# Optimization experiments

Measured on AMD Instinct MI355X. Metric: run time of the kernel, lower is better.

The kernel has to match this reference:

```python
import jax, jax.numpy as jnp
import numpy as np
from jax import lax


def setup_inputs() -> dict:
    key = jax.random.key(0)
    k1, k2, k3, k4 = jax.random.split(key, 4)
    B, C_in, H, W = 16, 64, 256, 256
    E, C_out, KH, KW = 4, 64, 3, 3
    inputs = jax.random.normal(k1, (B, C_in, H, W), dtype=jnp.float32)
    weight = jax.random.normal(k2, (E, C_out, C_in, KH, KW), dtype=jnp.float32) * 0.05
    fc_w = jax.random.normal(k3, (E, C_in), dtype=jnp.float32) * 0.1
    fc_b = jax.random.normal(k4, (E,), dtype=jnp.float32) * 0.1
    return {
        "inputs": inputs,
        "weight": weight,
        "fc_w": fc_w,
        "fc_b": fc_b,
        "stride": 1,
        "dilation": 1,
        "padding": 1,
    }


def reference(inputs, weight, fc_w, fc_b, stride, dilation, padding):
    # inputs: [B, C_in, H, W]; weight: [E, C_out, C_in, KH, KW]
    # Routing: adaptive avg pool to 1x1 == spatial mean, then Linear -> sigmoid.
    # (Dropout is identity in eval mode.)
    pooled = jnp.mean(inputs, axis=(2, 3))                      # [B, C_in]
    routing = jax.nn.sigmoid(pooled @ fc_w.T + fc_b)            # [B, E]
    # Per-sample mixed kernels.
    kernels = jnp.einsum("be,eoikl->boikl", routing, weight)    # [B, C_out, C_in, KH, KW]

    def conv_one(x, k):
        # x: [C_in, H, W], k: [C_out, C_in, KH, KW]
        y = lax.conv_general_dilated(
            x[None],
            k,
            window_strides=(stride, stride),
            padding=[(padding, padding), (padding, padding)],
            rhs_dilation=(dilation, dilation),
            dimension_numbers=("NCHW", "OIHW", "NCHW"),
        )
        return y[0]

    return jax.vmap(conv_one)(inputs, kernels)                  # [B, C_out, H', W']
```

## Files before the change

kernel.cpp:

```cpp
#include <hip/hip_runtime.h>
#include <math.h>

#define B_   16
#define CIN  64
#define COUT 64
#define H_   256
#define W_   256

typedef short s16x8  __attribute__((ext_vector_type(8)));
typedef float f32x16 __attribute__((ext_vector_type(16)));

__device__ __forceinline__ void split_bf16(float v, unsigned short& hi, unsigned short& lo) {
    unsigned u = __float_as_uint(v);
    hi = (unsigned short)(u >> 16);
    float hif = __uint_as_float(u & 0xffff0000u);
    lo = (unsigned short)(__float_as_uint(v - hif) >> 16);
}

__global__ __launch_bounds__(256) void pool_kernel(const float* __restrict__ x,
                                                   float* __restrict__ pooled) {
    const int plane = blockIdx.x;
    const float4* p = (const float4*)(x + (size_t)plane * (H_ * W_));
    float s = 0.f;
    for (int i = threadIdx.x; i < (H_ * W_) / 4; i += 256) {
        float4 v = p[i];
        s += (v.x + v.y) + (v.z + v.w);
    }
    #pragma unroll
    for (int off = 32; off > 0; off >>= 1) s += __shfl_down(s, off);
    __shared__ float red[4];
    if ((threadIdx.x & 63) == 0) red[threadIdx.x >> 6] = s;
    __syncthreads();
    if (threadIdx.x == 0)
        pooled[plane] = (red[0] + red[1] + red[2] + red[3]) * (1.f / (H_ * W_));
}

__global__ void routing_kernel(const float* __restrict__ pooled,
                               const float* __restrict__ fc_w,
                               const float* __restrict__ fc_b,
                               float* __restrict__ routing) {
    const int tid = threadIdx.x;
    const int b = tid >> 2, e = tid & 3;
    float s = fc_b[e];
    for (int c = 0; c < CIN; ++c) s += pooled[b * CIN + c] * fc_w[e * CIN + c];
    routing[b * 4 + e] = 1.f / (1.f + expf(-s));
}

__global__ __launch_bounds__(256) void mix_kernel(const float* __restrict__ routing,
                                                  const float* __restrict__ weight,
                                                  unsigned short* __restrict__ mixed) {
    const int gid = blockIdx.x * 256 + threadIdx.x;
    const int icL = gid & 15;
    const int oc  = (gid >> 4) & 63;
    const int q   = (gid >> 10) & 3;
    const int b   = gid >> 12;
    const int ic  = q * 16 + icL;

    float r[4];
    #pragma unroll
    for (int e = 0; e < 4; ++e) r[e] = routing[b * 4 + e];

    float s[9];
    #pragma unroll
    for (int t = 0; t < 9; ++t) s[t] = 0.f;
    #pragma unroll
    for (int e = 0; e < 4; ++e) {
        const float* wp = weight + (((size_t)e * COUT + oc) * CIN + ic) * 9;
        #pragma unroll
        for (int t = 0; t < 9; ++t) s[t] = fmaf(r[e], wp[t], s[t]);
    }
    unsigned short* base = mixed + (size_t)(b * 4 + q) * 18432;
    const int mb = oc >> 5;
    const int l  = (oc & 31) + ((icL >> 3) << 5);
    const int j  = icL & 7;
    #pragma unroll
    for (int t = 0; t < 9; ++t) {
        unsigned short hi, lo;
        split_bf16(s[t], hi, lo);
        base[(t * 4 + 0 + mb) * 512 + l * 8 + j] = hi;
        base[(t * 4 + 2 + mb) * 512 + l * 8 + j] = lo;
    }
}

__global__ __launch_bounds__(256, 3) void conv_kernel(const float* __restrict__ x,
                                                      const unsigned short* __restrict__ wmix,
                                                      float* __restrict__ y) {
    __shared__ __align__(16) unsigned short in_hi[10 * 34 * 16];
    __shared__ __align__(16) unsigned short in_lo[10 * 34 * 16];

    const int tid  = threadIdx.x;
    const int lane = tid & 63;
    const int wv   = tid >> 6;
    const int n    = lane & 31;
    const int kseg = lane >> 5;

    const int w0 = blockIdx.x * 32;
    const int h0 = blockIdx.y * 8;
    const int b  = blockIdx.z;

    const int p0 = tid;
    const int r0 = p0 / 34, c0 = p0 - r0 * 34;
    const int p1 = tid + 256;
    const int r1 = p1 / 34, c1 = p1 - r1 * 34;
    const bool has1 = (p1 < 340);

    const int gh0 = h0 - 1 + r0, gw0 = w0 - 1 + c0;
    const int gh1 = h0 - 1 + r1, gw1 = w0 - 1 + c1;
    const bool ok0 = ((unsigned)gh0 < H_) && ((unsigned)gw0 < W_);
    const bool ok1 = has1 && ((unsigned)gh1 < H_) && ((unsigned)gw1 < W_);

    const float* xb = x + (size_t)b * CIN * H_ * W_;
    const float* g0 = xb + (ok0 ? (gh0 * W_ + gw0) : 0);
    const float* g1 = xb + (ok1 ? (gh1 * W_ + gw1) : 0);

    float xr0[16], xr1[16];

    #define LOAD16(dst, gp, okf, qq) do {                                   \
        const float* _p = (gp) + (size_t)(qq) * 16 * (H_ * W_);             \
        _Pragma("unroll")                                                   \
        for (int _i = 0; _i < 16; ++_i)                                     \
            dst[_i] = (okf) ? _p[(size_t)_i * (H_ * W_)] : 0.f;             \
    } while (0)

    #define STAGE(pp, regs) do {                                            \
        s16x8 _vh0, _vh1, _vl0, _vl1;                                       \
        _Pragma("unroll")                                                   \
        for (int _i = 0; _i < 8; ++_i) {                                    \
            unsigned short _h, _l;                                          \
            split_bf16(regs[_i], _h, _l);                                   \
            _vh0[_i] = (short)_h; _vl0[_i] = (short)_l;                     \
            split_bf16(regs[8 + _i], _h, _l);                               \
            _vh1[_i] = (short)_h; _vl1[_i] = (short)_l;                     \
        }                                                                   \
        const int _c0 = (pp) * 2, _c1 = (pp) * 2 + 1;                       \
        const int _s0 = _c0 ^ ((_c0 >> 3) & 7);                             \
        const int _s1 = _c1 ^ ((_c1 >> 3) & 7);                             \
        ((s16x8*)in_hi)[_s0] = _vh0; ((s16x8*)in_hi)[_s1] = _vh1;           \
        ((s16x8*)in_lo)[_s0] = _vl0; ((s16x8*)in_lo)[_s1] = _vl1;           \
    } while (0)

    f32x16 acc[2][2];
    #pragma unroll
    for (int mb = 0; mb < 2; ++mb)
        #pragma unroll
        for (int nb = 0; nb < 2; ++nb)
            #pragma unroll
            for (int j = 0; j < 16; ++j) acc[mb][nb][j] = 0.f;

    const unsigned short* wb = wmix + (size_t)b * 4 * 18432 + lane * 8;

    LOAD16(xr0, g0, ok0, 0);
    if (has1) LOAD16(xr1, g1, ok1, 0);

    #pragma unroll 1
    for (int q = 0; q < 4; ++q) {
        __syncthreads();
        STAGE(p0, xr0);
        if (has1) STAGE(p1, xr1);
        __syncthreads();
        if (q < 3) {
            LOAD16(xr0, g0, ok0, q + 1);
            if (has1) LOAD16(xr1, g1, ok1, q + 1);
        }
        const unsigned short* wq = wb + q * 18432;

        s16x8 aH[2][2], aL[2][2];
        #pragma unroll
        for (int mb = 0; mb < 2; ++mb) {
            aH[0][mb] = *(const s16x8*)(wq + (0 + mb) * 512);
            aL[0][mb] = *(const s16x8*)(wq + (2 + mb) * 512);
        }
        #pragma unroll
        for (int tap = 0; tap < 9; ++tap) {
            const int cur = tap & 1, nxt = cur ^ 1;
            if (tap < 8) {
                #pragma unroll
                for (int mb = 0; mb < 2; ++mb) {
                    aH[nxt][mb] = *(const s16x8*)(wq + ((tap + 1) * 4 + 0 + mb) * 512);
                    aL[nxt][mb] = *(const s16x8*)(wq + ((tap + 1) * 4 + 2 + mb) * 512);
                }
            }
            const int kh = tap / 3, kw = tap - kh * 3;
            #pragma unroll
            for (int nb = 0; nb < 2; ++nb) {
                const int rin = wv * 2 + nb + kh;
                const int c   = (rin * 34 + n + kw) * 2 + kseg;
                const int cs  = c ^ ((c >> 3) & 7);
                const s16x8 bhi = ((const s16x8*)in_hi)[cs];
                const s16x8 blo = ((const s16x8*)in_lo)[cs];
                #pragma unroll
                for (int mb = 0; mb < 2; ++mb) {
                    acc[mb][nb] = __builtin_amdgcn_mfma_f32_32x32x16_bf16(aH[cur][mb], bhi, acc[mb][nb], 0, 0, 0);
                    acc[mb][nb] = __builtin_amdgcn_mfma_f32_32x32x16_bf16(aL[cur][mb], bhi, acc[mb][nb], 0, 0, 0);
                    acc[mb][nb] = __builtin_amdgcn_mfma_f32_32x32x16_bf16(aH[cur][mb], blo, acc[mb][nb], 0, 0, 0);
                }
            }
        }
    }

    #pragma unroll
    for (int mb = 0; mb < 2; ++mb) {
        #pragma unroll
        for (int nb = 0; nb < 2; ++nb) {
            const int hrow = h0 + wv * 2 + nb;
            #pragma unroll
            for (int r = 0; r < 16; ++r) {
                const int oc = mb * 32 + (r & 3) + 8 * (r >> 2) + 4 * kseg;
                y[(((size_t)b * COUT + oc) * H_ + hrow) * W_ + w0 + n] = acc[mb][nb][r];
            }
        }
    }
}

extern "C" void kernel_launch(void* const* d_in, const int* in_sizes, int n_in,
                              void* d_out, int out_size, void* d_ws, size_t ws_size,
                              hipStream_t stream) {
    const float* x      = (const float*)d_in[0];
    const float* weight = (const float*)d_in[1];
    const float* fc_w   = (const float*)d_in[2];
    const float* fc_b   = (const float*)d_in[3];
    float* out = (float*)d_out;

    float* ws      = (float*)d_ws;
    float* pooled  = ws;
    float* routing = ws + 1024;
    unsigned short* mixed = (unsigned short*)(ws + 1088);

    pool_kernel<<<B_ * CIN, 256, 0, stream>>>(x, pooled);
    routing_kernel<<<1, 64, 0, stream>>>(pooled, fc_w, fc_b, routing);
    mix_kernel<<<(B_ * 4 * COUT * 16) / 256, 256, 0, stream>>>(routing, weight, mixed);

    dim3 grid(W_ / 32, H_ / 8, B_);
    conv_kernel<<<grid, 256, 0, stream>>>(x, mixed, out);
}
```

Measured before the change: 644.9 us.

## Reuse LDS rows across kh taps, remap grid for XCD locality, drop prefetch

Restructures the conv inner loop by kw so the four input rows read from LDS are reused across all three kh taps, cutting LDS reads. The LDS layout becomes planar (hi/lo by k-segment) without the XOR swizzle. A 1D grid is remapped so consecutive blocks on each XCD cover adjacent tiles of the same batch. The register prefetch of the next channel group is removed and occupancy bounds drop from 3 to 2 waves per EU, which frees registers but exposes global load latency and may add LDS bank conflicts.

After: 640.2 us. No clear change (-0.7%).

```diff
diff --git a/kernel.cpp b/kernel.cpp
--- a/kernel.cpp
+++ b/kernel.cpp
@@ -82,11 +82,10 @@
     }
 }
 
-__global__ __launch_bounds__(256, 3) void conv_kernel(const float* __restrict__ x,
+__global__ __launch_bounds__(256, 2) void conv_kernel(const float* __restrict__ x,
                                                       const unsigned short* __restrict__ wmix,
                                                       float* __restrict__ y) {
-    __shared__ __align__(16) unsigned short in_hi[10 * 34 * 16];
-    __shared__ __align__(16) unsigned short in_lo[10 * 34 * 16];
+    __shared__ __align__(16) unsigned short in_s[4 * 340 * 8];
 
     const int tid  = threadIdx.x;
     const int lane = tid & 63;
@@ -94,9 +93,11 @@
     const int n    = lane & 31;
     const int kseg = lane >> 5;
 
-    const int w0 = blockIdx.x * 32;
-    const int h0 = blockIdx.y * 8;
-    const int b  = blockIdx.z;
+    const int bid = blockIdx.x;
+    const int wg  = (bid & 7) * 512 + (bid >> 3);
+    const int w0 = (wg & 7) * 32;
+    const int h0 = ((wg >> 3) & 31) * 8;
+    const int b  = wg >> 8;
 
     const int p0 = tid;
     const int r0 = p0 / 34, c0 = p0 - r0 * 34;
@@ -112,8 +113,6 @@
     const float* xb = x + (size_t)b * CIN * H_ * W_;
     const float* g0 = xb + (ok0 ? (gh0 * W_ + gw0) : 0);
     const float* g1 = xb + (ok1 ? (gh1 * W_ + gw1) : 0);
-
-    float xr0[16], xr1[16];
 
     #define LOAD16(dst, gp, okf, qq) do {                                   \
         const float* _p = (gp) + (size_t)(qq) * 16 * (H_ * W_);             \
@@ -123,20 +122,19 @@
     } while (0)
 
     #define STAGE(pp, regs) do {                                            \
-        s16x8 _vh0, _vh1, _vl0, _vl1;                                       \
+        s16x8 _h0, _h1, _l0, _l1;                                           \
         _Pragma("unroll")                                                   \
         for (int _i = 0; _i < 8; ++_i) {                                    \
             unsigned short _h, _l;                                          \
             split_bf16(regs[_i], _h, _l);                                   \
-            _vh0[_i] = (short)_h; _vl0[_i] = (short)_l;                     \
+            _h0[_i] = (short)_h; _l0[_i] = (short)_l;                       \
             split_bf16(regs[8 + _i], _h, _l);                               \
-            _vh1[_i] = (short)_h; _vl1[_i] = (short)_l;                     \
+            _h1[_i] = (short)_h; _l1[_i] = (short)_l;                       \
         }                                                                   \
-        const int _c0 = (pp) * 2, _c1 = (pp) * 2 + 1;                       \
-        const int _s0 = _c0 ^ ((_c0 >> 3) & 7);                             \
-        const int _s1 = _c1 ^ ((_c1 >> 3) & 7);                             \
-        ((s16x8*)in_hi)[_s0] = _vh0; ((s16x8*)in_hi)[_s1] = _vh1;           \
-        ((s16x8*)in_lo)[_s0] = _vl0; ((s16x8*)in_lo)[_s1] = _vl1;           \
+        ((s16x8*)in_s)[0 * 340 + (pp)] = _h0;                               \
+        ((s16x8*)in_s)[1 * 340 + (pp)] = _h1;                               \
+        ((s16x8*)in_s)[2 * 340 + (pp)] = _l0;                               \
+        ((s16x8*)in_s)[3 * 340 + (pp)] = _l1;                               \
     } while (0)
 
     f32x16 acc[2][2];
@@ -148,51 +146,49 @@
             for (int j = 0; j < 16; ++j) acc[mb][nb][j] = 0.f;
 
     const unsigned short* wb = wmix + (size_t)b * 4 * 18432 + lane * 8;
-
-    LOAD16(xr0, g0, ok0, 0);
-    if (has1) LOAD16(xr1, g1, ok1, 0);
 
     #pragma unroll 1
     for (int q = 0; q < 4; ++q) {
         __syncthreads();
-        STAGE(p0, xr0);
-        if (has1) STAGE(p1, xr1);
+        {
+            float xr[16];
+            LOAD16(xr, g0, ok0, q);
+            STAGE(p0, xr);
+            if (has1) { LOAD16(xr, g1, ok1, q); STAGE(p1, xr); }
+        }
         __syncthreads();
-        if (q < 3) {
-            LOAD16(xr0, g0, ok0, q + 1);
-            if (has1) LOAD16(xr1, g1, ok1, q + 1);
-        }
         const unsigned short* wq = wb + q * 18432;
 
-        s16x8 aH[2][2], aL[2][2];
-        #pragma unroll
-        for (int mb = 0; mb < 2; ++mb) {
-            aH[0][mb] = *(const s16x8*)(wq + (0 + mb) * 512);
-            aL[0][mb] = *(const s16x8*)(wq + (2 + mb) * 512);
-        }
-        #pragma unroll
-        for (int tap = 0; tap < 9; ++tap) {
-            const int cur = tap & 1, nxt = cur ^ 1;
-            if (tap < 8) {
+        #pragma unroll
+        for (int kw = 0; kw < 3; ++kw) {
+            s16x8 aH[3][2], aL[3][2];
+            #pragma unroll
+            for (int kh = 0; kh < 3; ++kh) {
+                const int tap = kh * 3 + kw;
                 #pragma unroll
                 for (int mb = 0; mb < 2; ++mb) {
-                    aH[nxt][mb] = *(const s16x8*)(wq + ((tap + 1) * 4 + 0 + mb) * 512);
-                    aL[nxt][mb] = *(const s16x8*)(wq + ((tap + 1) * 4 + 2 + mb) * 512);
+                    aH[kh][mb] = *(const s16x8*)(wq + (tap * 4 + 0 + mb) * 512);
+                    aL[kh][mb] = *(const s16x8*)(wq + (tap * 4 + 2 + mb) * 512);
                 }
             }
-            const int kh = tap / 3, kw = tap - kh * 3;
-            #pragma unroll
-            for (int nb = 0; nb < 2; ++nb) {
-                const int rin = wv * 2 + nb + kh;
-                const int c   = (rin * 34 + n + kw) * 2 + kseg;
-                const int cs  = c ^ ((c >> 3) & 7);
-                const s16x8 bhi = ((const s16x8*)in_hi)[cs];
-                const s16x8 blo = ((const s16x8*)in_lo)[cs];
+            s16x8 bh[4], bl[4];
+            #pragma unroll
+            for (int r = 0; r < 4; ++r) {
+                const int pos = (wv * 2 + r) * 34 + n + kw;
+                bh[r] = ((const s16x8*)in_s)[(0 + kseg) * 340 + pos];
+                bl[r] = ((const s16x8*)in_s)[(2 + kseg) * 340 + pos];
+            }
+            #pragma unroll
+            for (int kh = 0; kh < 3; ++kh) {
                 #pragma unroll
-                for (int mb = 0; mb < 2; ++mb) {
-                    acc[mb][nb] = __builtin_amdgcn_mfma_f32_32x32x16_bf16(aH[cur][mb], bhi, acc[mb][nb], 0, 0, 0);
-                    acc[mb][nb] = __builtin_amdgcn_mfma_f32_32x32x16_bf16(aL[cur][mb], bhi, acc[mb][nb], 0, 0, 0);
-                    acc[mb][nb] = __builtin_amdgcn_mfma_f32_32x32x16_bf16(aH[cur][mb], blo, acc[mb][nb], 0, 0, 0);
+                for (int nb = 0; nb < 2; ++nb) {
+                    const int r = nb + kh;
+                    #pragma unroll
+                    for (int mb = 0; mb < 2; ++mb) {
+                        acc[mb][nb] = __builtin_amdgcn_mfma_f32_32x32x16_bf16(aH[kh][mb], bh[r], acc[mb][nb], 0, 0, 0);
+                        acc[mb][nb] = __builtin_amdgcn_mfma_f32_32x32x16_bf16(aL[kh][mb], bh[r], acc[mb][nb], 0, 0, 0);
+                        acc[mb][nb] = __builtin_amdgcn_mfma_f32_32x32x16_bf16(aH[kh][mb], bl[r], acc[mb][nb], 0, 0, 0);
+                    }
                 }
             }
         }
@@ -230,6 +226,5 @@
     routing_kernel<<<1, 64, 0, stream>>>(pooled, fc_w, fc_b, routing);
     mix_kernel<<<(B_ * 4 * COUT * 16) / 256, 256, 0, stream>>>(routing, weight, mixed);
 
-    dim3 grid(W_ / 32, H_ / 8, B_);
-    conv_kernel<<<grid, 256, 0, stream>>>(x, mixed, out);
-}
+    conv_kernel<<<4096, 256, 0, stream>>>(x, mixed, out);
+}
```
